# Performance work log

Measured on AMD Instinct MI355X. Metric: run time of the kernel, lower is better.

Reference implementation:

```python
import jax, jax.numpy as jnp
import numpy as np

K = 8
HID = 32
BOUND = 5.0
SIGMA_MIN = 1e-4
MIN_DERIV = 1e-3
B, T, C = 32, 4096, 512


def setup_inputs() -> dict:
    key = jax.random.key(0)
    k1, k2, k3 = jax.random.split(key, 3)
    x = jax.random.normal(k1, (B, T, C), jnp.float32)
    W1 = jax.random.normal(k2, (HID, 2), jnp.float32) * 0.5
    b1 = jnp.zeros((HID,), jnp.float32)
    W2 = jax.random.normal(k3, (3 * K + 1, HID), jnp.float32) * 0.1
    b2 = jnp.zeros((3 * K + 1,), jnp.float32)
    return {"x": x, "W1": W1, "b1": b1, "W2": W2, "b2": b2}


def _rqs_forward(x2d, kx, ky, d):
    # x2d: (BC, T); kx, ky, d: (BC, K+1)
    w = kx[:, 1:] - kx[:, :-1]
    h = ky[:, 1:] - ky[:, :-1]
    s = h / jnp.maximum(w, 1e-8)
    idx = jax.vmap(lambda a, v: jnp.searchsorted(a, v, side='right'))(kx, x2d) - 1
    idx = jnp.clip(idx, 0, K - 1)  # (BC, T)
    g = lambda t, i: jnp.take_along_axis(t, i, axis=1)
    w_k = g(w, idx)
    h_k = g(h, idx)
    s_k = g(s, idx)
    d_k = g(d, idx)
    d_k1 = g(d, jnp.minimum(idx + 1, K))
    kx_l = g(kx, idx)
    ky_l = g(ky, idx)
    zeta = jnp.clip((x2d - kx_l) / jnp.maximum(w_k, 1e-8), 0.0, 1.0)
    numer = h_k * (s_k * zeta * zeta + d_k * zeta * (1.0 - zeta))
    denom = s_k + (d_k1 + d_k - 2.0 * s_k) * zeta * (1.0 - zeta)
    z2d = ky_l + numer / jnp.maximum(denom, 1e-8)
    tail = (x2d < -BOUND) | (x2d > BOUND)
    return jnp.where(tail, x2d, z2d)


def reference(x, W1, b1, W2, b2):
    Bb, Tt, Cc = x.shape
    # affine standardisation (unbiased std matching torch.std default)
    mu = jnp.mean(x, axis=1, keepdims=True)
    sig = jnp.maximum(jnp.std(x, axis=1, ddof=1, keepdims=True), SIGMA_MIN)
    z_pre = (x - mu) / sig  # (B, T, C)
    zd = jax.lax.stop_gradient(z_pre)
    skew = jnp.mean(zd ** 3, axis=1)          # (B, C)
    ekurt = jnp.mean(zd ** 4, axis=1) - 3.0   # (B, C)
    stats = jnp.stack([skew, ekurt], axis=-1).reshape(Bb * Cc, 2)
    hid = jax.nn.relu(stats @ W1.T + b1)
    raw = hid @ W2.T + b2                      # (BC, 3K+1)
    widths = jax.nn.softmax(raw[:, :K], axis=-1) * (2.0 * BOUND)
    heights = jax.nn.softmax(raw[:, K:2 * K], axis=-1) * (2.0 * BOUND)
    derivs = jax.nn.softplus(raw[:, 2 * K:]) + MIN_DERIV  # (BC, K+1)
    pad = jnp.full((widths.shape[0], 1), -BOUND, widths.dtype)
    kx = jnp.concatenate([pad, -BOUND + jnp.cumsum(widths, axis=-1)], axis=-1)
    ky = jnp.concatenate([pad, -BOUND + jnp.cumsum(heights, axis=-1)], axis=-1)
    x2d = jnp.transpose(z_pre, (0, 2, 1)).reshape(Bb * Cc, Tt)
    z2d = _rqs_forward(x2d, kx, ky, derivs)
    return jnp.transpose(z2d.reshape(Bb, Cc, Tt), (0, 2, 1))
```

## Files before the change

### kernel.cpp

```cpp
#include <hip/hip_runtime.h>
#include <math.h>

#define KNOTS 8
#define HIDN 32
#define TT 4096
#define CC 512
#define NB 32
#define BOUNDF 5.0f
#define CT 32
#define NTG 16
#define TPT (TT / NTG)

__global__ __launch_bounds__(512, 4)
void k_fused(const float* __restrict__ x, const float* __restrict__ W1,
             const float* __restrict__ b1, const float* __restrict__ W2,
             const float* __restrict__ b2, float* __restrict__ out)
{
    const int bb = blockIdx.y;
    const int c0 = blockIdx.x * CT;
    const int ci = threadIdx.x & (CT - 1);
    const int tg = threadIdx.x >> 5;

    __shared__ float red[NTG][4][CT];
    __shared__ float mom[4][CT];
    __shared__ float pA[CT], pB[CT];
    __shared__ float pKx[7][CT];
    __shared__ float2 bZ[KNOTS][CT];
    __shared__ float2 bY[KNOTS][CT];
    __shared__ float2 bD[KNOTS][CT];

    const size_t base = (size_t)bb * TT * CC + c0 + ci;
    const float* pxt = x + base + (size_t)tg * CC;

    float s1 = 0.f, s2 = 0.f, s3 = 0.f, s4 = 0.f;
    #pragma unroll 8
    for (int k = 0; k < TPT; ++k) {
        float v  = pxt[(size_t)k * (NTG * CC)];
        float v2 = v * v;
        s1 += v;
        s2 = fmaf(v,  v,  s2);
        s3 = fmaf(v2, v,  s3);
        s4 = fmaf(v2, v2, s4);
    }
    red[tg][0][ci] = s1; red[tg][1][ci] = s2;
    red[tg][2][ci] = s3; red[tg][3][ci] = s4;
    __syncthreads();

    if (threadIdx.x < 4 * CT) {
        const int m = threadIdx.x >> 5, c = threadIdx.x & (CT - 1);
        float acc = 0.f;
        #pragma unroll
        for (int g = 0; g < NTG; ++g) acc += red[g][m][c];
        mom[m][c] = acc;
    }
    __syncthreads();

    if (threadIdx.x < CT) {
        const int c = threadIdx.x;
        const float n  = (float)TT;
        const float t1 = mom[0][c], t2 = mom[1][c], t3 = mom[2][c], t4 = mom[3][c];
        const float mu  = t1 / n;
        const float ex2 = t2 / n, ex3 = t3 / n, ex4 = t4 / n;
        float var = (t2 - n * mu * mu) / (n - 1.f);
        var = fmaxf(var, 0.f);
        const float sig  = fmaxf(sqrtf(var), 1e-4f);
        const float inv  = 1.f / sig;
        const float mu2  = mu * mu;
        const float ez3  = ex3 - 3.f * mu * ex2 + 2.f * mu * mu2;
        const float ez4  = ex4 - 4.f * mu * ex3 + 6.f * mu2 * ex2 - 3.f * mu2 * mu2;
        const float inv2 = inv * inv;
        const float skew  = ez3 * inv2 * inv;
        const float ekurt = ez4 * inv2 * inv2 - 3.f;

        float hid[HIDN];
        #pragma unroll
        for (int h = 0; h < HIDN; ++h) {
            float v = fmaf(W1[2*h], skew, fmaf(W1[2*h+1], ekurt, b1[h]));
            hid[h] = fmaxf(v, 0.f);
        }

        float e[KNOTS], kxr[KNOTS+1], kyr[KNOTS+1], dr[KNOTS+1];
        {
            float mx = -1e30f;
            #pragma unroll
            for (int o = 0; o < KNOTS; ++o) {
                float acc = b2[o];
                #pragma unroll
                for (int h = 0; h < HIDN; ++h) acc = fmaf(W2[o*HIDN + h], hid[h], acc);
                e[o] = acc; mx = fmaxf(mx, acc);
            }
            float sum = 0.f;
            #pragma unroll
            for (int o = 0; o < KNOTS; ++o) { e[o] = expf(e[o] - mx); sum += e[o]; }
            const float scale = (2.f * BOUNDF) / sum;
            float cum = -BOUNDF; kxr[0] = -BOUNDF;
            #pragma unroll
            for (int o = 0; o < KNOTS; ++o) { cum = fmaf(e[o], scale, cum); kxr[o+1] = cum; }
        }
        {
            float mx = -1e30f;
            #pragma unroll
            for (int o = 0; o < KNOTS; ++o) {
                float acc = b2[KNOTS + o];
                #pragma unroll
                for (int h = 0; h < HIDN; ++h) acc = fmaf(W2[(KNOTS+o)*HIDN + h], hid[h], acc);
                e[o] = acc; mx = fmaxf(mx, acc);
            }
            float sum = 0.f;
            #pragma unroll
            for (int o = 0; o < KNOTS; ++o) { e[o] = expf(e[o] - mx); sum += e[o]; }
            const float scale = (2.f * BOUNDF) / sum;
            float cum = -BOUNDF; kyr[0] = -BOUNDF;
            #pragma unroll
            for (int o = 0; o < KNOTS; ++o) { cum = fmaf(e[o], scale, cum); kyr[o+1] = cum; }
        }
        #pragma unroll
        for (int o = 0; o < KNOTS+1; ++o) {
            float acc = b2[2*KNOTS + o];
            #pragma unroll
            for (int h = 0; h < HIDN; ++h) acc = fmaf(W2[(2*KNOTS+o)*HIDN + h], hid[h], acc);
            float sp = fmaxf(acc, 0.f) + log1pf(expf(-fabsf(acc)));
            dr[o] = sp + 1e-3f;
        }

        pA[c] = inv;
        pB[c] = -mu * inv;
        #pragma unroll
        for (int j = 1; j <= 7; ++j) pKx[j-1][c] = kxr[j];
        #pragma unroll
        for (int j = 0; j < KNOTS; ++j) {
            const float w    = kxr[j+1] - kxr[j];
            const float wm   = fmaxf(w, 1e-8f);
            const float invw = 1.f / wm;
            const float h    = kyr[j+1] - kyr[j];
            bZ[j][c] = make_float2(-kxr[j] * invw, invw);
            bY[j][c] = make_float2(kyr[j], h);
            bD[j][c] = make_float2(dr[j], dr[j] + dr[j+1]);
        }
    }
    __syncthreads();

    const float a  = pA[ci];
    const float bz = pB[ci];
    const float kx1 = pKx[0][ci], kx2 = pKx[1][ci], kx3 = pKx[2][ci],
                kx4 = pKx[3][ci], kx5 = pKx[4][ci], kx6 = pKx[5][ci],
                kx7 = pKx[6][ci];
    float* pot = out + base + (size_t)tg * CC;

    for (int kb = TPT / 8 - 1; kb >= 0; --kb) {
        float xv[8];
        #pragma unroll
        for (int j = 0; j < 8; ++j)
            xv[j] = pxt[(size_t)(kb * 8 + j) * (NTG * CC)];
        #pragma unroll
        for (int j = 0; j < 8; ++j) {
            const float z = fmaf(xv[j], a, bz);
            const bool  c4 = z >= kx4;
            const float mB = c4 ? kx6 : kx2;
            const bool  cB = z >= mB;
            const float nLo = c4 ? kx5 : kx1;
            const float nHi = c4 ? kx7 : kx3;
            const float mC = cB ? nHi : nLo;
            const bool  cC = z >= mC;
            const int off = (c4 ? 4*CT : 0) + (cB ? 2*CT : 0) + (cC ? CT : 0) + ci;

            const float2 Z = ((const float2*)bZ)[off];
            const float2 Y = ((const float2*)bY)[off];
            const float2 D = ((const float2*)bD)[off];

            const float zeta = fmaf(z, Z.y, Z.x);
            const float u    = fmaf(-zeta, zeta, zeta);
            const float s    = Y.y * Z.y;
            const float R    = fmaf(-2.f, s, D.y);
            const float den  = fmaf(R, u, s);
            const float inner= fmaf(s * zeta, zeta, D.x * u);
            const float res  = fmaf(Y.y * inner,
                                    __builtin_amdgcn_rcpf(fmaxf(den, 1e-8f)), Y.x);
            const float o = (fabsf(z) > BOUNDF) ? z : res;
            __builtin_nontemporal_store(o, &pot[(size_t)(kb * 8 + j) * (NTG * CC)]);
        }
    }
}

extern "C" void kernel_launch(void* const* d_in, const int* in_sizes, int n_in,
                              void* d_out, int out_size, void* d_ws, size_t ws_size,
                              hipStream_t stream) {
    const float* x  = (const float*)d_in[0];
    const float* W1 = (const float*)d_in[1];
    const float* b1 = (const float*)d_in[2];
    const float* W2 = (const float*)d_in[3];
    const float* b2 = (const float*)d_in[4];
    float* out = (float*)d_out;

    k_fused<<<dim3(CC / CT, NB), dim3(512), 0, stream>>>(x, W1, b1, W2, b2, out);
}
```

Measured before the change: 128.8 us.

## Vectorize channel access to float2 per thread with even/odd parameter tables

Each thread now handles two adjacent channels using 8-byte float2 loads and stores, with 16 channel lanes and 32 time groups per block instead of 32 lanes and 16 groups. The reduction and the spline parameter tables are split into even and odd channel copies so each lane reads its own entries. The aim is fewer, wider global memory instructions and more independent work per thread. In exchange each thread keeps two sets of knots, which raises register pressure, and the wave's 8-byte accesses span only 128-byte row segments.

```diff
diff --git a/kernel.cpp b/kernel.cpp
--- a/kernel.cpp
+++ b/kernel.cpp
@@ -8,8 +8,42 @@
 #define NB 32
 #define BOUNDF 5.0f
 #define CT 32
-#define NTG 16
+#define CL 16
+#define NTG 32
 #define TPT (TT / NTG)
+#define ROWS2 (CC / 2)
+
+typedef float f32x2 __attribute__((ext_vector_type(2)));
+
+
+__device__ __forceinline__ float rqs_one(float z,
+    float k1, float k2, float k3, float k4, float k5, float k6, float k7,
+    const f32x2* __restrict__ bZ, const f32x2* __restrict__ bY,
+    const f32x2* __restrict__ bD, int lc)
+{
+    const bool  c4 = z >= k4;
+    const float mB = c4 ? k6 : k2;
+    const bool  cB = z >= mB;
+    const float nLo = c4 ? k5 : k1;
+    const float nHi = c4 ? k7 : k3;
+    const float mC = cB ? nHi : nLo;
+    const bool  cC = z >= mC;
+    const int off = (c4 ? 4*CL : 0) + (cB ? 2*CL : 0) + (cC ? CL : 0) + lc;
+
+    const f32x2 Z = bZ[off];
+    const f32x2 Y = bY[off];
+    const f32x2 D = bD[off];
+
+    const float zeta = fmaf(z, Z.y, Z.x);
+    const float u    = fmaf(-zeta, zeta, zeta);
+    const float s    = Y.y * Z.y;
+    const float R    = fmaf(-2.f, s, D.y);
+    const float den  = fmaf(R, u, s);
+    const float inner= fmaf(s * zeta, zeta, D.x * u);
+    const float res  = fmaf(Y.y * inner,
+                            __builtin_amdgcn_rcpf(fmaxf(den, 1e-8f)), Y.x);
+    return (fabsf(z) > BOUNDF) ? z : res;
+}
 
 __global__ __launch_bounds__(512, 4)
 void k_fused(const float* __restrict__ x, const float* __restrict__ W1,
@@ -18,40 +52,45 @@
 {
     const int bb = blockIdx.y;
     const int c0 = blockIdx.x * CT;
-    const int ci = threadIdx.x & (CT - 1);
-    const int tg = threadIdx.x >> 5;
-
-    __shared__ float red[NTG][4][CT];
+    const int lc = threadIdx.x & (CL - 1);
+    const int tg = threadIdx.x >> 4;
+
+    __shared__ f32x2 red2[NTG][4][CL];
     __shared__ float mom[4][CT];
     __shared__ float pA[CT], pB[CT];
     __shared__ float pKx[7][CT];
-    __shared__ float2 bZ[KNOTS][CT];
-    __shared__ float2 bY[KNOTS][CT];
-    __shared__ float2 bD[KNOTS][CT];
-
-    const size_t base = (size_t)bb * TT * CC + c0 + ci;
-    const float* pxt = x + base + (size_t)tg * CC;
-
-    float s1 = 0.f, s2 = 0.f, s3 = 0.f, s4 = 0.f;
+    __shared__ f32x2 bZe[KNOTS][CL], bZo[KNOTS][CL];
+    __shared__ f32x2 bYe[KNOTS][CL], bYo[KNOTS][CL];
+    __shared__ f32x2 bDe[KNOTS][CL], bDo[KNOTS][CL];
+
+    const size_t base2 = ((size_t)bb * TT * CC + c0) / 2 + lc + (size_t)tg * ROWS2;
+    const f32x2* pxt = (const f32x2*)x + base2;
+
+    float s1e = 0.f, s2e = 0.f, s3e = 0.f, s4e = 0.f;
+    float s1o = 0.f, s2o = 0.f, s3o = 0.f, s4o = 0.f;
     #pragma unroll 8
     for (int k = 0; k < TPT; ++k) {
-        float v  = pxt[(size_t)k * (NTG * CC)];
-        float v2 = v * v;
-        s1 += v;
-        s2 = fmaf(v,  v,  s2);
-        s3 = fmaf(v2, v,  s3);
-        s4 = fmaf(v2, v2, s4);
-    }
-    red[tg][0][ci] = s1; red[tg][1][ci] = s2;
-    red[tg][2][ci] = s3; red[tg][3][ci] = s4;
+        const f32x2 v = pxt[(size_t)k * (NTG * ROWS2)];
+        const float ve = v.x, vo = v.y;
+        const float ve2 = ve * ve, vo2 = vo * vo;
+        s1e += ve;                  s1o += vo;
+        s2e = fmaf(ve,  ve,  s2e);  s2o = fmaf(vo,  vo,  s2o);
+        s3e = fmaf(ve2, ve,  s3e);  s3o = fmaf(vo2, vo,  s3o);
+        s4e = fmaf(ve2, ve2, s4e);  s4o = fmaf(vo2, vo2, s4o);
+    }
+    red2[tg][0][lc] = (f32x2){s1e, s1o};
+    red2[tg][1][lc] = (f32x2){s2e, s2o};
+    red2[tg][2][lc] = (f32x2){s3e, s3o};
+    red2[tg][3][lc] = (f32x2){s4e, s4o};
     __syncthreads();
 
-    if (threadIdx.x < 4 * CT) {
-        const int m = threadIdx.x >> 5, c = threadIdx.x & (CT - 1);
-        float acc = 0.f;
-        #pragma unroll
-        for (int g = 0; g < NTG; ++g) acc += red[g][m][c];
-        mom[m][c] = acc;
+    if (threadIdx.x < 64) {
+        const int m = threadIdx.x >> 4, c = threadIdx.x & (CL - 1);
+        f32x2 acc = (f32x2){0.f, 0.f};
+        #pragma unroll
+        for (int g = 0; g < NTG; ++g) acc += red2[g][m][c];
+        mom[m][2*c]   = acc.x;
+        mom[m][2*c+1] = acc.y;
     }
     __syncthreads();
 
@@ -127,57 +166,49 @@
         pB[c] = -mu * inv;
         #pragma unroll
         for (int j = 1; j <= 7; ++j) pKx[j-1][c] = kxr[j];
+
+        const int  ch = c >> 1;
+        const bool odd = (c & 1) != 0;
         #pragma unroll
         for (int j = 0; j < KNOTS; ++j) {
             const float w    = kxr[j+1] - kxr[j];
             const float wm   = fmaxf(w, 1e-8f);
             const float invw = 1.f / wm;
             const float h    = kyr[j+1] - kyr[j];
-            bZ[j][c] = make_float2(-kxr[j] * invw, invw);
-            bY[j][c] = make_float2(kyr[j], h);
-            bD[j][c] = make_float2(dr[j], dr[j] + dr[j+1]);
+            const f32x2 Z = {-kxr[j] * invw, invw};
+            const f32x2 Y = {kyr[j], h};
+            const f32x2 D = {dr[j], dr[j] + dr[j+1]};
+            if (odd) { bZo[j][ch] = Z; bYo[j][ch] = Y; bDo[j][ch] = D; }
+            else     { bZe[j][ch] = Z; bYe[j][ch] = Y; bDe[j][ch] = D; }
         }
     }
     __syncthreads();
 
-    const float a  = pA[ci];
-    const float bz = pB[ci];
-    const float kx1 = pKx[0][ci], kx2 = pKx[1][ci], kx3 = pKx[2][ci],
-                kx4 = pKx[3][ci], kx5 = pKx[4][ci], kx6 = pKx[5][ci],
-                kx7 = pKx[6][ci];
-    float* pot = out + base + (size_t)tg * CC;
+    const float aE = pA[2*lc],   aO = pA[2*lc+1];
+    const float bE = pB[2*lc],   bO = pB[2*lc+1];
+    const float e1 = pKx[0][2*lc], e2 = pKx[1][2*lc], e3 = pKx[2][2*lc],
+                e4 = pKx[3][2*lc], e5 = pKx[4][2*lc], e6 = pKx[5][2*lc],
+                e7 = pKx[6][2*lc];
+    const float o1 = pKx[0][2*lc+1], o2 = pKx[1][2*lc+1], o3 = pKx[2][2*lc+1],
+                o4 = pKx[3][2*lc+1], o5 = pKx[4][2*lc+1], o6 = pKx[5][2*lc+1],
+                o7 = pKx[6][2*lc+1];
+    f32x2* pot = (f32x2*)out + base2;
 
     for (int kb = TPT / 8 - 1; kb >= 0; --kb) {
-        float xv[8];
+        f32x2 xv[8];
         #pragma unroll
         for (int j = 0; j < 8; ++j)
-            xv[j] = pxt[(size_t)(kb * 8 + j) * (NTG * CC)];
+            xv[j] = pxt[(size_t)(kb * 8 + j) * (NTG * ROWS2)];
         #pragma unroll
         for (int j = 0; j < 8; ++j) {
-            const float z = fmaf(xv[j], a, bz);
-            const bool  c4 = z >= kx4;
-            const float mB = c4 ? kx6 : kx2;
-            const bool  cB = z >= mB;
-            const float nLo = c4 ? kx5 : kx1;
-            const float nHi = c4 ? kx7 : kx3;
-            const float mC = cB ? nHi : nLo;
-            const bool  cC = z >= mC;
-            const int off = (c4 ? 4*CT : 0) + (cB ? 2*CT : 0) + (cC ? CT : 0) + ci;
-
-            const float2 Z = ((const float2*)bZ)[off];
-            const float2 Y = ((const float2*)bY)[off];
-            const float2 D = ((const float2*)bD)[off];
-
-            const float zeta = fmaf(z, Z.y, Z.x);
-            const float u    = fmaf(-zeta, zeta, zeta);
-            const float s    = Y.y * Z.y;
-            const float R    = fmaf(-2.f, s, D.y);
-            const float den  = fmaf(R, u, s);
-            const float inner= fmaf(s * zeta, zeta, D.x * u);
-            const float res  = fmaf(Y.y * inner,
-                                    __builtin_amdgcn_rcpf(fmaxf(den, 1e-8f)), Y.x);
-            const float o = (fabsf(z) > BOUNDF) ? z : res;
-            __builtin_nontemporal_store(o, &pot[(size_t)(kb * 8 + j) * (NTG * CC)]);
+            const float zE = fmaf(xv[j].x, aE, bE);
+            const float zO = fmaf(xv[j].y, aO, bO);
+            const float rE = rqs_one(zE, e1,e2,e3,e4,e5,e6,e7,
+                                     &bZe[0][0], &bYe[0][0], &bDe[0][0], lc);
+            const float rO = rqs_one(zO, o1,o2,o3,o4,o5,o6,o7,
+                                     &bZo[0][0], &bYo[0][0], &bDo[0][0], lc);
+            const f32x2 r = {rE, rO};
+            __builtin_nontemporal_store(r, &pot[(size_t)(kb * 8 + j) * (NTG * ROWS2)]);
         }
     }
 }
```

Result: no change. 131.1 us (+1.8%).
